# Optimization experiments

Measured on AMD Instinct MI355X. Metric: run time of the kernel, lower is better.

Reference implementation:

```python
import jax, jax.numpy as jnp
import numpy as np

EPS = 1e-6
SCALING = 32 ** -0.5  # key_dim ** -0.5


def _ln(x, g, b):
    m = jnp.mean(x, -1, keepdims=True)
    v = jnp.var(x, -1, keepdims=True)
    return (x - m) * jax.lax.rsqrt(v + EPS) * g + b


def _dwconv(x, w, b, pad):
    # x: (B,H,W,C); w: (kh,kw,1,C) depthwise kernel
    y = jax.lax.conv_general_dilated(
        x, w, (1, 1), [(pad, pad), (pad, pad)],
        dimension_numbers=("NHWC", "HWIO", "NHWC"),
        feature_group_count=x.shape[-1])
    return y + b


def _rotate_every_two(x):
    x1 = x[..., ::2]
    x2 = x[..., 1::2]
    return jnp.stack([-x2, x1], axis=-1).reshape(x.shape)


def _theta_shift(x, sin, cos):
    return x * cos + _rotate_every_two(x) * sin


def setup_inputs() -> dict:
    key = jax.random.key(0)
    ks = jax.random.split(key, 32)
    B, H, W, C = 2, 56, 56, 256
    N, D = 8, C // 8          # heads, key_dim
    F = 1024                  # ffn_dim
    L = H * W
    g = 2 ** -2.5
    inp = {
        "x": jax.random.normal(ks[0], (B, H, W, C), jnp.float32),
        "sin": jax.random.normal(ks[1], (H, W, D), jnp.float32),
        "cos": jax.random.normal(ks[2], (H, W, D), jnp.float32),
        "mask": jax.random.normal(ks[3], (N, L, L), jnp.float32),
        # pos dwconv 3x3
        "pos_w": jax.random.normal(ks[4], (3, 3, 1, C), jnp.float32) * 0.05,
        "pos_b": jnp.zeros((C,), jnp.float32),
        # retention layernorm
        "ln1_g": jnp.ones((C,), jnp.float32),
        "ln1_b": jnp.zeros((C,), jnp.float32),
        # q/k/v projections (stored as (in,out))
        "wq": jax.random.normal(ks[5], (C, C), jnp.float32) * g * (2.0 / (C + C)) ** 0.5 * 10,
        "bq": jnp.zeros((C,), jnp.float32),
        "wk": jax.random.normal(ks[6], (C, C), jnp.float32) * g * 0.06,
        "bk": jnp.zeros((C,), jnp.float32),
        "wv": jax.random.normal(ks[7], (C, C), jnp.float32) * g * 0.06,
        "bv": jnp.zeros((C,), jnp.float32),
        # lepe dwconv 5x5
        "lepe_w": jax.random.normal(ks[8], (5, 5, 1, C), jnp.float32) * 0.05,
        "lepe_b": jnp.zeros((C,), jnp.float32),
        # out proj
        "wo": jax.random.normal(ks[9], (C, C), jnp.float32) * 0.06,
        "bo": jnp.zeros((C,), jnp.float32),
        # final layernorm
        "ln2_g": jnp.ones((C,), jnp.float32),
        "ln2_b": jnp.zeros((C,), jnp.float32),
        # ffn
        "w1": jax.random.normal(ks[10], (C, F), jnp.float32) * 0.04,
        "b1": jnp.zeros((F,), jnp.float32),
        "ffn_w": jax.random.normal(ks[11], (3, 3, 1, F), jnp.float32) * 0.05,
        "ffn_b": jnp.zeros((F,), jnp.float32),
        "w2": jax.random.normal(ks[12], (F, C), jnp.float32) * 0.04,
        "b2": jnp.zeros((C,), jnp.float32),
    }
    return inp


def _forward(x, sin, cos, mask, pos_w, pos_b, ln1_g, ln1_b, wq, bq, wk, bk,
             wv, bv, lepe_w, lepe_b, wo, bo, ln2_g, ln2_b, w1, b1,
             ffn_w, ffn_b, w2, b2):
    B, H, W, C = x.shape
    N = mask.shape[0]
    D = C // N
    L = H * W

    # positional dwconv residual
    x = x + _dwconv(x, pos_w, pos_b, 1)

    # ---- retention (VisionRetentionAll) ----
    y = _ln(x, ln1_g, ln1_b)
    q = y @ wq + bq
    k = (y @ wk + bk) * SCALING
    v = y @ wv + bv
    lepe = _dwconv(v, lepe_w, lepe_b, 2)

    # (B,H,W,C) -> (B,N,H,W,D)
    q = q.reshape(B, H, W, N, D).transpose(0, 3, 1, 2, 4)
    k = k.reshape(B, H, W, N, D).transpose(0, 3, 1, 2, 4)
    qr = _theta_shift(q, sin, cos).reshape(B, N, L, D)
    kr = _theta_shift(k, sin, cos).reshape(B, N, L, D)
    vr = v.reshape(B, H, W, N, D).transpose(0, 3, 1, 2, 4).reshape(B, N, L, D)

    qk = jnp.einsum("bnld,bnmd->bnlm", qr, kr) + mask  # (B,N,L,L)
    att = jax.nn.softmax(qk, axis=-1)
    out = jnp.einsum("bnlm,bnmd->bnld", att, vr)       # (B,N,L,D)
    out = out.transpose(0, 2, 1, 3).reshape(B, H, W, C)
    out = (out + lepe) @ wo + bo
    x = x + out

    # ---- FFN with depthwise conv ----
    z = _ln(x, ln2_g, ln2_b)
    z = jax.nn.gelu(z @ w1 + b1, approximate=False)
    z = z + _dwconv(z, ffn_w, ffn_b, 1)
    z = z @ w2 + b2
    return x + z


def reference(x, sin, cos, mask, pos_w, pos_b, ln1_g, ln1_b, wq, bq, wk, bk,
              wv, bv, lepe_w, lepe_b, wo, bo, ln2_g, ln2_b, w1, b1,
              ffn_w, ffn_b, w2, b2):
    return _forward(x, sin, cos, mask, pos_w, pos_b, ln1_g, ln1_b, wq, bq,
                    wk, bk, wv, bv, lepe_w, lepe_b, wo, bo, ln2_g, ln2_b,
                    w1, b1, ffn_w, ffn_b, w2, b2)
```

## Files before the change

kernel.cpp:

```cpp
#include <hip/hip_runtime.h>
#include <hip/hip_bf16.h>
#include <math.h>

#define Bn 2
#define Hn 56
#define Wn 56
#define Cn 256
#define Nh 8
#define Dh 32
#define Fn 1024
#define Ln (Hn*Wn)
#define Mrows (Bn*Ln)
#define SCALING_K 0.17677669529663687f

typedef __attribute__((ext_vector_type(4))) float f32x4;
typedef __attribute__((ext_vector_type(8))) short s16x8;
typedef unsigned short ushort_t;

__device__ __forceinline__ ushort_t f2bf(float f) {
    __hip_bfloat16 h = __float2bfloat16(f);
    return *reinterpret_cast<ushort_t*>(&h);
}

#define GLOAD16(gp, sp) __builtin_amdgcn_global_load_lds( \
    (const __attribute__((address_space(1))) void*)(gp), \
    (__attribute__((address_space(3))) void*)(sp), 16, 0, 0)

__global__ __launch_bounds__(256) void transpose_w(
    const float* __restrict__ wq, const float* __restrict__ wk, const float* __restrict__ wv,
    const float* __restrict__ wo, const float* __restrict__ w1, const float* __restrict__ w2,
    ushort_t* __restrict__ wqkvT, ushort_t* __restrict__ woT,
    ushort_t* __restrict__ w1T, ushort_t* __restrict__ w2T)
{
    int z = blockIdx.z;
    const float* src; ushort_t* dst; int K, N; float scale = 1.f;
    switch (z) {
      case 0: src=wq; dst=wqkvT;           K=256;  N=256;  break;
      case 1: src=wk; dst=wqkvT+256*256;   K=256;  N=256;  scale=SCALING_K; break;
      case 2: src=wv; dst=wqkvT+512*256;   K=256;  N=256;  break;
      case 3: src=wo; dst=woT;             K=256;  N=256;  break;
      case 4: src=w1; dst=w1T;             K=256;  N=1024; break;
      default: src=w2; dst=w2T;            K=1024; N=256;  break;
    }
    int n0 = blockIdx.x << 5, k0 = blockIdx.y << 5;
    if (n0 >= N || k0 >= K) return;
    __shared__ float tile[32][33];
    int tx = threadIdx.x & 31, ty = threadIdx.x >> 5;
    #pragma unroll
    for (int r = 0; r < 4; ++r)
        tile[ty + 8*r][tx] = src[(size_t)(k0 + ty + 8*r)*N + n0 + tx] * scale;
    __syncthreads();
    #pragma unroll
    for (int r = 0; r < 4; ++r)
        dst[(size_t)(n0 + ty + 8*r)*K + k0 + tx] = f2bf(tile[tx][ty + 8*r]);
}

__global__ void prep_bias(const float* __restrict__ bq, const float* __restrict__ bk,
                          const float* __restrict__ bv, float* __restrict__ bqkv)
{
    int i = blockIdx.x*256 + threadIdx.x;
    if (i < 768)
        bqkv[i] = (i < 256) ? bq[i] : (i < 512 ? bk[i-256]*SCALING_K : bv[i-512]);
}

__global__ __launch_bounds__(256) void dwconv_ln(
    const float* __restrict__ x, const float* __restrict__ wgt, const float* __restrict__ bias,
    const float* __restrict__ lng, const float* __restrict__ lnb,
    float* __restrict__ out, ushort_t* __restrict__ ybf)
{
    int t = threadIdx.x;
    int cg = t & 63;
    int g = blockIdx.x*4 + (t >> 6);
    int w0 = (g % 14) << 2;
    int hr = g / 14;
    int h = hr % Hn;
    int c = cg << 2;
    float4 wv9[9];
    #pragma unroll
    for (int i = 0; i < 9; ++i) wv9[i] = *(const float4*)&wgt[i*Cn + c];
    float4 bias4 = *(const float4*)&bias[c];
    float4 acc[4] = {bias4, bias4, bias4, bias4};
    const float* base = x + (size_t)(hr - h)*Wn*Cn + c;
    #pragma unroll
    for (int dh = 0; dh < 3; ++dh) {
        int hh = h + dh - 1;
        if (hh < 0 || hh >= Hn) continue;
        const float* rowp = base + (size_t)hh*Wn*Cn;
        float4 xv[6];
        #pragma unroll
        for (int j = 0; j < 6; ++j) {
            int wc = w0 - 1 + j;
            xv[j] = (wc >= 0 && wc < Wn) ? *(const float4*)&rowp[(size_t)wc*Cn]
                                         : make_float4(0.f,0.f,0.f,0.f);
        }
        #pragma unroll
        for (int dw = 0; dw < 3; ++dw) {
            float4 wv = wv9[dh*3 + dw];
            #pragma unroll
            for (int p = 0; p < 4; ++p) {
                acc[p].x += xv[p+dw].x*wv.x; acc[p].y += xv[p+dw].y*wv.y;
                acc[p].z += xv[p+dw].z*wv.z; acc[p].w += xv[p+dw].w*wv.w;
            }
        }
        if (dh == 1) {
            #pragma unroll
            for (int p = 0; p < 4; ++p) {
                acc[p].x += xv[p+1].x; acc[p].y += xv[p+1].y;
                acc[p].z += xv[p+1].z; acc[p].w += xv[p+1].w;
            }
        }
    }
    float s[4], q[4];
    #pragma unroll
    for (int p = 0; p < 4; ++p) {
        s[p] = acc[p].x + acc[p].y + acc[p].z + acc[p].w;
        q[p] = acc[p].x*acc[p].x + acc[p].y*acc[p].y + acc[p].z*acc[p].z + acc[p].w*acc[p].w;
    }
    #pragma unroll
    for (int m = 1; m < 64; m <<= 1) {
        #pragma unroll
        for (int p = 0; p < 4; ++p) {
            s[p] += __shfl_xor(s[p], m);
            q[p] += __shfl_xor(q[p], m);
        }
    }
    float4 g4 = *(const float4*)&lng[c];
    float4 b4 = *(const float4*)&lnb[c];
    size_t pixbase = (size_t)hr*Wn + w0;
    #pragma unroll
    for (int p = 0; p < 4; ++p) {
        *(float4*)&out[(pixbase + p)*Cn + c] = acc[p];
        float mean = s[p] * (1.0f/Cn);
        float rstd = rsqrtf(q[p] * (1.0f/Cn) - mean*mean + 1e-6f);
        ushort_t o[4] = {
            f2bf((acc[p].x - mean)*rstd*g4.x + b4.x),
            f2bf((acc[p].y - mean)*rstd*g4.y + b4.y),
            f2bf((acc[p].z - mean)*rstd*g4.z + b4.z),
            f2bf((acc[p].w - mean)*rstd*g4.w + b4.w)
        };
        *(uint2*)&ybf[(pixbase + p)*Cn + c] = *(uint2*)o;
    }
}

template<int KS, int OBF>
__global__ __launch_bounds__(256) void dwconv4(
    const float* __restrict__ in, const float* __restrict__ wgt, const float* __restrict__ bias,
    void* __restrict__ outv, int C, int inld, int addin)
{
    constexpr int PAD = KS/2;
    int t = threadIdx.x;
    int cgs = C >> 2;
    int qpb = 256 / cgs;
    int cg = t % cgs;
    int g = blockIdx.x*qpb + t/cgs;
    int w0 = (g % 14) << 2;
    int hr = g / 14;
    int h = hr % Hn;
    int c = cg << 2;
    float4 bias4 = *(const float4*)&bias[c];
    float4 acc[4] = {bias4, bias4, bias4, bias4};
    const float* base = in + (size_t)(hr - h)*Wn*inld + c;
    #pragma unroll
    for (int dh = 0; dh < KS; ++dh) {
        int hh = h + dh - PAD;
        if (hh < 0 || hh >= Hn) continue;
        const float* rowp = base + (size_t)hh*Wn*inld;
        float4 xv[KS+3];
        #pragma unroll
        for (int j = 0; j < KS+3; ++j) {
            int wc = w0 - PAD + j;
            xv[j] = (wc >= 0 && wc < Wn) ? *(const float4*)&rowp[(size_t)wc*inld]
                                         : make_float4(0.f,0.f,0.f,0.f);
        }
        #pragma unroll
        for (int dw = 0; dw < KS; ++dw) {
            float4 wv = *(const float4*)&wgt[(dh*KS + dw)*C + c];
            #pragma unroll
            for (int p = 0; p < 4; ++p) {
                acc[p].x += xv[p+dw].x*wv.x; acc[p].y += xv[p+dw].y*wv.y;
                acc[p].z += xv[p+dw].z*wv.z; acc[p].w += xv[p+dw].w*wv.w;
            }
        }
        if (addin && dh == PAD) {
            #pragma unroll
            for (int p = 0; p < 4; ++p) {
                acc[p].x += xv[p+PAD].x; acc[p].y += xv[p+PAD].y;
                acc[p].z += xv[p+PAD].z; acc[p].w += xv[p+PAD].w;
            }
        }
    }
    size_t pixbase = (size_t)hr*Wn + w0;
    if (OBF) {
        ushort_t* outb = (ushort_t*)outv;
        #pragma unroll
        for (int p = 0; p < 4; ++p) {
            ushort_t tmp[4] = { f2bf(acc[p].x), f2bf(acc[p].y), f2bf(acc[p].z), f2bf(acc[p].w) };
            *(uint2*)&outb[(pixbase + p)*C + c] = *(uint2*)tmp;
        }
    } else {
        float* outf = (float*)outv;
        #pragma unroll
        for (int p = 0; p < 4; ++p)
            *(float4*)&outf[(pixbase + p)*C + c] = acc[p];
    }
}

__global__ __launch_bounds__(256) void ln_apply(
    const float* __restrict__ in, const float* __restrict__ g, const float* __restrict__ b,
    ushort_t* __restrict__ out)
{
    int t = threadIdx.x;
    int lane = t & 63;
    int row = blockIdx.x*4 + (t >> 6);
    int c = lane << 2;
    float4 v = *(const float4*)&in[(size_t)row*Cn + c];
    float s1 = v.x + v.y + v.z + v.w;
    float s2 = v.x*v.x + v.y*v.y + v.z*v.z + v.w*v.w;
    #pragma unroll
    for (int m = 1; m < 64; m <<= 1) {
        s1 += __shfl_xor(s1, m);
        s2 += __shfl_xor(s2, m);
    }
    float mean = s1 * (1.0f/Cn);
    float rstd = rsqrtf(s2 * (1.0f/Cn) - mean*mean + 1e-6f);
    float4 g4 = *(const float4*)&g[c];
    float4 b4 = *(const float4*)&b[c];
    ushort_t o[4] = {
        f2bf((v.x - mean)*rstd*g4.x + b4.x),
        f2bf((v.y - mean)*rstd*g4.y + b4.y),
        f2bf((v.z - mean)*rstd*g4.z + b4.z),
        f2bf((v.w - mean)*rstd*g4.w + b4.w)
    };
    *(uint2*)&out[(size_t)row*Cn + c] = *(uint2*)o;
}

__global__ __launch_bounds__(256) void gemm_bf16(
    const ushort_t* __restrict__ A, int lda,
    const ushort_t* __restrict__ BT, const float* __restrict__ bias,
    const float* __restrict__ resid, float* __restrict__ out, int ldo,
    int K, int gelu_flag)
{
    __shared__ __align__(16) ushort_t As[64*64];
    __shared__ __align__(16) ushort_t Bs[64*64];
    int t = threadIdx.x;
    int wid = t >> 6, lane = t & 63, l16 = lane & 15, quad = lane >> 4;
    int n0 = blockIdx.x << 6, m0 = blockIdx.y << 6;
    int rl = lane >> 3;
    int swc = ((lane & 7) ^ rl) << 3;
    const ushort_t* aA = A  + (size_t)(m0 + wid*8 + rl)*lda + swc;
    const ushort_t* aB = BT + (size_t)(n0 + wid*8 + rl)*K   + swc;
    int x7 = l16 & 7;
    f32x4 acc[4] = {{0,0,0,0},{0,0,0,0},{0,0,0,0},{0,0,0,0}};
    for (int k0 = 0; k0 < K; k0 += 64) {
        __syncthreads();
        GLOAD16(aA + k0,                 &As[wid*512]);
        GLOAD16(aA + k0 + (size_t)32*lda, &As[2048 + wid*512]);
        GLOAD16(aB + k0,                 &Bs[wid*512]);
        GLOAD16(aB + k0 + (size_t)32*K,   &Bs[2048 + wid*512]);
        __syncthreads();
        #pragma unroll
        for (int kk = 0; kk < 2; ++kk) {
            int ch = (((kk << 2) | quad) ^ x7) << 3;
            s16x8 af = *(const s16x8*)&As[(wid*16 + l16)*64 + ch];
            #pragma unroll
            for (int j = 0; j < 4; ++j) {
                s16x8 bf = *(const s16x8*)&Bs[(j*16 + l16)*64 + ch];
                acc[j] = __builtin_amdgcn_mfma_f32_16x16x32_bf16(af, bf, acc[j], 0, 0, 0);
            }
        }
    }
    #pragma unroll
    for (int j = 0; j < 4; ++j) {
        int col = n0 + j*16 + l16;
        float bv = bias[col];
        #pragma unroll
        for (int r = 0; r < 4; ++r) {
            int row = m0 + wid*16 + quad*4 + r;
            float v = acc[j][r] + bv;
            if (gelu_flag) v = 0.5f * v * (1.0f + erff(v * 0.70710678118654752f));
            size_t off = (size_t)row*ldo + col;
            if (resid) v += resid[off];
            out[off] = v;
        }
    }
}

__global__ __launch_bounds__(256) void pack_qkv(
    const float* __restrict__ qkv,
    const float* __restrict__ sp, const float* __restrict__ cp,
    ushort_t* __restrict__ qb, ushort_t* __restrict__ kb, ushort_t* __restrict__ vbT)
{
    __shared__ __align__(16) ushort_t Vl[64][40];
    int t = threadIdx.x;
    int l0 = blockIdx.x << 6;
    int n = blockIdx.y;
    int b = blockIdx.z;
    {
        int ll = t >> 2, dc = (t & 3) << 3;
        int l = l0 + ll;
        size_t gbase = ((size_t)(b*Ln + l))*768 + n*Dh + dc;
        float qx[8], kx[8], vx[8], sv[8], cv[8];
        *(float4*)&qx[0] = *(const float4*)&qkv[gbase];
        *(float4*)&qx[4] = *(const float4*)&qkv[gbase+4];
        *(float4*)&kx[0] = *(const float4*)&qkv[gbase+256];
        *(float4*)&kx[4] = *(const float4*)&qkv[gbase+260];
        *(float4*)&vx[0] = *(const float4*)&qkv[gbase+512];
        *(float4*)&vx[4] = *(const float4*)&qkv[gbase+516];
        size_t scb = (size_t)l*Dh + dc;
        *(float4*)&sv[0] = *(const float4*)&sp[scb];
        *(float4*)&sv[4] = *(const float4*)&sp[scb+4];
        *(float4*)&cv[0] = *(const float4*)&cp[scb];
        *(float4*)&cv[4] = *(const float4*)&cp[scb+4];
        ushort_t qo[8], ko[8], vo[8];
        #pragma unroll
        for (int j = 0; j < 8; j += 2) {
            float q0 = qx[j]*cv[j] - qx[j+1]*sv[j];
            float q1 = qx[j+1]*cv[j+1] + qx[j]*sv[j+1];
            float k0 = kx[j]*cv[j] - kx[j+1]*sv[j];
            float k1 = kx[j+1]*cv[j+1] + kx[j]*sv[j+1];
            qo[j] = f2bf(q0); qo[j+1] = f2bf(q1);
            ko[j] = f2bf(k0); ko[j+1] = f2bf(k1);
            vo[j] = f2bf(vx[j]); vo[j+1] = f2bf(vx[j+1]);
        }
        size_t hbase = ((size_t)((b*Nh + n)*Ln + l))*Dh + dc;
        *(uint4*)&qb[hbase] = *(uint4*)qo;
        *(uint4*)&kb[hbase] = *(uint4*)ko;
        *(uint4*)&Vl[ll][dc] = *(uint4*)vo;
    }
    __syncthreads();
    {
        int d = t >> 3, lc = (t & 7) << 3;
        ushort_t tmp[8];
        #pragma unroll
        for (int i = 0; i < 8; ++i) tmp[i] = Vl[lc + i][d];
        size_t tbase = ((size_t)((b*Nh + n)*Dh + d))*Ln + l0 + lc;
        *(uint4*)&vbT[tbase] = *(uint4*)tmp;
    }
}

__global__ __launch_bounds__(512) void flash_mfma(
    const ushort_t* __restrict__ qb, const ushort_t* __restrict__ kb,
    const ushort_t* __restrict__ vbT, const float* __restrict__ mask,
    const float* __restrict__ lepe, ushort_t* __restrict__ out)
{
    __shared__ __align__(16) ushort_t Kt[2][64][40];
    __shared__ __align__(16) ushort_t Vt[2][32][72];
    __shared__ __align__(16) ushort_t Ps[8][16][72];
    int t = threadIdx.x;
    int wid = t >> 6, lane = t & 63, l16 = lane & 15, quad = lane >> 4;
    int bb = wid & 1, wq16 = wid >> 1;
    int l0 = blockIdx.x << 6;
    int n = blockIdx.y;

    const ushort_t* qbp = qb + ((size_t)(bb*Nh + n))*Ln*Dh;
    s16x8 qfrag = *(const s16x8*)(qbp + (size_t)(l0 + wq16*16 + l16)*Dh + quad*8);
    const float* mbase = mask + (size_t)n*Ln*Ln + (size_t)(l0 + wq16*16 + quad*4)*Ln;

    int sb   = t >> 8;
    int krow = (t >> 2) & 63, kkc = (t & 3) << 3;
    int vrow = (t >> 3) & 31, vkc = (t & 7) << 3;
    const ushort_t* kst = kb  + ((size_t)(sb*Nh + n))*Ln*Dh;
    const ushort_t* vst = vbT + ((size_t)((sb*Nh + n)*Dh + vrow))*Ln;

    f32x4 O0 = {0.f,0.f,0.f,0.f}, O1 = {0.f,0.f,0.f,0.f};
    float m_[4], l_[4];
    #pragma unroll
    for (int r = 0; r < 4; ++r) { m_[r] = -INFINITY; l_[r] = 0.f; }

    uint4 kreg = *(const uint4*)(kst + (size_t)krow*Dh + kkc);
    uint4 vreg = *(const uint4*)(vst + vkc);
    f32x4 c0, c1, c2, c3;
    #pragma unroll
    for (int r = 0; r < 4; ++r) {
        const float* mr = mbase + (size_t)r*Ln + l16;
        c0[r] = mr[0]; c1[r] = mr[16]; c2[r] = mr[32]; c3[r] = mr[48];
    }

    for (int m0 = 0; m0 < Ln; m0 += 64) {
        __syncthreads();
        *(uint4*)&Kt[sb][krow][kkc] = kreg;
        *(uint4*)&Vt[sb][vrow][vkc] = vreg;
        __syncthreads();

        int m1 = m0 + 64;
        uint4 krn = kreg, vrn = vreg;
        f32x4 d0 = c0, d1 = c1, d2 = c2, d3 = c3;
        if (m1 < Ln) {
            krn = *(const uint4*)(kst + (size_t)(m1 + krow)*Dh + kkc);
            vrn = *(const uint4*)(vst + m1 + vkc);
            #pragma unroll
            for (int r = 0; r < 4; ++r) {
                const float* mr = mbase + (size_t)r*Ln + m1 + l16;
                d0[r] = mr[0]; d1[r] = mr[16]; d2[r] = mr[32]; d3[r] = mr[48];
            }
        }

        f32x4 S[4];
        {
            s16x8 kf0 = *(const s16x8*)&Kt[bb][ 0 + l16][quad*8];
            s16x8 kf1 = *(const s16x8*)&Kt[bb][16 + l16][quad*8];
            s16x8 kf2 = *(const s16x8*)&Kt[bb][32 + l16][quad*8];
            s16x8 kf3 = *(const s16x8*)&Kt[bb][48 + l16][quad*8];
            S[0] = __builtin_amdgcn_mfma_f32_16x16x32_bf16(qfrag, kf0, c0, 0, 0, 0);
            S[1] = __builtin_amdgcn_mfma_f32_16x16x32_bf16(qfrag, kf1, c1, 0, 0, 0);
            S[2] = __builtin_amdgcn_mfma_f32_16x16x32_bf16(qfrag, kf2, c2, 0, 0, 0);
            S[3] = __builtin_amdgcn_mfma_f32_16x16x32_bf16(qfrag, kf3, c3, 0, 0, 0);
        }
        #pragma unroll
        for (int r = 0; r < 4; ++r) {
            float tm = fmaxf(fmaxf(S[0][r], S[1][r]), fmaxf(S[2][r], S[3][r]));
            tm = fmaxf(tm, __shfl_xor(tm, 1));
            tm = fmaxf(tm, __shfl_xor(tm, 2));
            tm = fmaxf(tm, __shfl_xor(tm, 4));
            tm = fmaxf(tm, __shfl_xor(tm, 8));
            float nm = fmaxf(m_[r], tm);
            float al = __expf(m_[r] - nm);
            m_[r] = nm;
            float p0 = __expf(S[0][r] - nm);
            float p1 = __expf(S[1][r] - nm);
            float p2 = __expf(S[2][r] - nm);
            float p3 = __expf(S[3][r] - nm);
            float ps = p0 + p1 + p2 + p3;
            ps += __shfl_xor(ps, 1); ps += __shfl_xor(ps, 2);
            ps += __shfl_xor(ps, 4); ps += __shfl_xor(ps, 8);
            l_[r] = l_[r]*al + ps;
            O0[r] *= al; O1[r] *= al;
            int rr = quad*4 + r;
            Ps[wid][rr][ 0 + l16] = f2bf(p0);
            Ps[wid][rr][16 + l16] = f2bf(p1);
            Ps[wid][rr][32 + l16] = f2bf(p2);
            Ps[wid][rr][48 + l16] = f2bf(p3);
        }
        #pragma unroll
        for (int kc = 0; kc < 2; ++kc) {
            s16x8 pf  = *(const s16x8*)&Ps[wid][l16][kc*32 + quad*8];
            s16x8 vf0 = *(const s16x8*)&Vt[bb][ 0 + l16][kc*32 + quad*8];
            s16x8 vf1 = *(const s16x8*)&Vt[bb][16 + l16][kc*32 + quad*8];
            O0 = __builtin_amdgcn_mfma_f32_16x16x32_bf16(pf, vf0, O0, 0, 0, 0);
            O1 = __builtin_amdgcn_mfma_f32_16x16x32_bf16(pf, vf1, O1, 0, 0, 0);
        }
        kreg = krn; vreg = vrn;
        c0 = d0; c1 = d1; c2 = d2; c3 = d3;
    }
    #pragma unroll
    for (int r = 0; r < 4; ++r) {
        float inv = 1.0f / l_[r];
        size_t row = (size_t)(bb*Ln + l0 + wq16*16 + quad*4 + r)*Cn + n*Dh;
        out[row + l16]      = f2bf(O0[r] * inv + lepe[row + l16]);
        out[row + 16 + l16] = f2bf(O1[r] * inv + lepe[row + 16 + l16]);
    }
}

extern "C" void kernel_launch(void* const* d_in, const int* in_sizes, int n_in,
                              void* d_out, int out_size, void* d_ws, size_t ws_size,
                              hipStream_t stream) {
    const float* x     = (const float*)d_in[0];
    const float* sinp  = (const float*)d_in[1];
    const float* cosp  = (const float*)d_in[2];
    const float* mask  = (const float*)d_in[3];
    const float* pos_w = (const float*)d_in[4];
    const float* pos_b = (const float*)d_in[5];
    const float* ln1_g = (const float*)d_in[6];
    const float* ln1_b = (const float*)d_in[7];
    const float* wq = (const float*)d_in[8];
    const float* bq = (const float*)d_in[9];
    const float* wk = (const float*)d_in[10];
    const float* bk = (const float*)d_in[11];
    const float* wv = (const float*)d_in[12];
    const float* bv = (const float*)d_in[13];
    const float* lepe_w = (const float*)d_in[14];
    const float* lepe_b = (const float*)d_in[15];
    const float* wo = (const float*)d_in[16];
    const float* bo = (const float*)d_in[17];
    const float* ln2_g = (const float*)d_in[18];
    const float* ln2_b = (const float*)d_in[19];
    const float* w1 = (const float*)d_in[20];
    const float* b1 = (const float*)d_in[21];
    const float* ffn_w = (const float*)d_in[22];
    const float* ffn_b = (const float*)d_in[23];
    const float* w2 = (const float*)d_in[24];
    const float* b2 = (const float*)d_in[25];

    float* ws = (float*)d_ws;
    const size_t MC = (size_t)Mrows*Cn;
    const size_t HC = MC/2;
    float* xbuf = ws;
    float* x2   = ws + MC;
    float* lepe = ws + 2*MC;
    ushort_t* ybf   = (ushort_t*)(ws + 3*MC);
    ushort_t* attbf = (ushort_t*)(ws + 3*MC + HC);
    ushort_t* zbf   = (ushort_t*)(ws + 4*MC);
    float* qkv = ws + 4*MC + HC;
    ushort_t* qb  = (ushort_t*)(ws + 7*MC + HC);
    ushort_t* kb  = (ushort_t*)(ws + 8*MC);
    ushort_t* vbT = (ushort_t*)(ws + 8*MC + HC);
    float* z1 = ws + 4*MC + HC;
    ushort_t* z2bf = (ushort_t*)(ws + 9*MC);
    float* wtb = ws + 11*MC;
    ushort_t* wqkvT = (ushort_t*)wtb;
    ushort_t* woT   = (ushort_t*)(wtb + 98304);
    ushort_t* w1T   = (ushort_t*)(wtb + 131072);
    ushort_t* w2T   = (ushort_t*)(wtb + 262144);
    float*    bqkv  = wtb + 393216;
    float* outp = (float*)d_out;

    transpose_w<<<dim3(32,32,6), 256, 0, stream>>>(wq,wk,wv,wo,w1,w2, wqkvT,woT,w1T,w2T);
    prep_bias<<<3, 256, 0, stream>>>(bq,bk,bv,bqkv);
    dwconv_ln<<<Mrows/16, 256, 0, stream>>>(x, pos_w, pos_b, ln1_g, ln1_b, xbuf, ybf);
    gemm_bf16<<<dim3(12, Mrows/64), 256, 0, stream>>>(ybf, Cn,
        wqkvT, bqkv, nullptr, qkv, 768, Cn, 0);
    pack_qkv<<<dim3(Ln/64, Nh, Bn), 256, 0, stream>>>(qkv, sinp, cosp, qb, kb, vbT);
    dwconv4<5,0><<<Mrows/16, 256, 0, stream>>>(qkv+512, lepe_w, lepe_b, lepe, Cn, 768, 0);
    flash_mfma<<<dim3(Ln/64, Nh), 512, 0, stream>>>(qb, kb, vbT, mask, lepe, attbf);
    gemm_bf16<<<dim3(4, Mrows/64), 256, 0, stream>>>(attbf, Cn,
        woT, bo, xbuf, x2, Cn, Cn, 0);
    ln_apply<<<Mrows/4, 256, 0, stream>>>(x2, ln2_g, ln2_b, zbf);
    gemm_bf16<<<dim3(16, Mrows/64), 256, 0, stream>>>(zbf, Cn,
        w1T, b1, nullptr, z1, Fn, Cn, 1);
    dwconv4<3,1><<<Mrows/4, 256, 0, stream>>>(z1, ffn_w, ffn_b, z2bf, Fn, Fn, 1);
    gemm_bf16<<<dim3(4, Mrows/64), 256, 0, stream>>>(z2bf, Fn,
        w2T, b2, x2, outp, Cn, Fn, 0);
}
```

Baseline: 629.2 us.

## Fuse rotary shift and Q/K packing into QKV GEMM epilogue

The QKV GEMM epilogue now applies bias, the rotary theta shift (pairing neighbouring columns via lane shuffles) and bf16 conversion, and writes Q and K directly in per-head layout. V is written as fp32 and packed by a smaller vpack kernel, which removes the fp32 768-wide qkv round trip. The bias-prep kernel is folded into the weight-transpose launch, and the flash kernel defers its row-sum shuffle reduction to the end instead of doing it every tile. In exchange, the epilogue stores are scattered 2-byte writes and sin/cos are gathered per element.

```diff
diff --git a/kernel.cpp b/kernel.cpp
--- a/kernel.cpp
+++ b/kernel.cpp
@@ -29,10 +29,18 @@
 __global__ __launch_bounds__(256) void transpose_w(
     const float* __restrict__ wq, const float* __restrict__ wk, const float* __restrict__ wv,
     const float* __restrict__ wo, const float* __restrict__ w1, const float* __restrict__ w2,
+    const float* __restrict__ bq, const float* __restrict__ bk, const float* __restrict__ bv,
     ushort_t* __restrict__ wqkvT, ushort_t* __restrict__ woT,
-    ushort_t* __restrict__ w1T, ushort_t* __restrict__ w2T)
+    ushort_t* __restrict__ w1T, ushort_t* __restrict__ w2T, float* __restrict__ bqkv)
 {
     int z = blockIdx.z;
+    if (z == 6) {
+        if (blockIdx.x == 0 && blockIdx.y == 0) {
+            for (int i = threadIdx.x; i < 768; i += 256)
+                bqkv[i] = (i < 256) ? bq[i] : (i < 512 ? bk[i-256]*SCALING_K : bv[i-512]);
+        }
+        return;
+    }
     const float* src; ushort_t* dst; int K, N; float scale = 1.f;
     switch (z) {
       case 0: src=wq; dst=wqkvT;           K=256;  N=256;  break;
@@ -53,14 +61,6 @@
     #pragma unroll
     for (int r = 0; r < 4; ++r)
         dst[(size_t)(n0 + ty + 8*r)*K + k0 + tx] = f2bf(tile[tx][ty + 8*r]);
-}
-
-__global__ void prep_bias(const float* __restrict__ bq, const float* __restrict__ bk,
-                          const float* __restrict__ bv, float* __restrict__ bqkv)
-{
-    int i = blockIdx.x*256 + threadIdx.x;
-    if (i < 768)
-        bqkv[i] = (i < 256) ? bq[i] : (i < 512 ? bk[i-256]*SCALING_K : bv[i-512]);
 }
 
 __global__ __launch_bounds__(256) void dwconv_ln(
@@ -238,7 +238,9 @@
     const ushort_t* __restrict__ A, int lda,
     const ushort_t* __restrict__ BT, const float* __restrict__ bias,
     const float* __restrict__ resid, float* __restrict__ out, int ldo,
-    int K, int gelu_flag)
+    int K, int epi,
+    ushort_t* __restrict__ qbo, ushort_t* __restrict__ kbo, float* __restrict__ vbo,
+    const float* __restrict__ sp, const float* __restrict__ cp)
 {
     __shared__ __align__(16) ushort_t As[64*64];
     __shared__ __align__(16) ushort_t Bs[64*64];
@@ -269,6 +271,37 @@
             }
         }
     }
+    if (epi == 2) {
+        #pragma unroll
+        for (int j = 0; j < 4; ++j) {
+            int col = n0 + j*16 + l16;
+            float bv = bias[col];
+            if (col < 512) {
+                int d = col & 31;
+                int hn = (col >> 5) & 7;
+                ushort_t* dst = (col < 256) ? qbo : kbo;
+                #pragma unroll
+                for (int r = 0; r < 4; ++r) {
+                    int row = m0 + wid*16 + quad*4 + r;
+                    float v = acc[j][r] + bv;
+                    float vp = __shfl_xor(v, 1);
+                    int b = (row >= Ln) ? 1 : 0;
+                    int ll = row - b*Ln;
+                    float cc = cp[ll*Dh + d];
+                    float ss = sp[ll*Dh + d];
+                    float o = (col & 1) ? (v*cc + vp*ss) : (v*cc - vp*ss);
+                    dst[(((size_t)(b*Nh + hn)*Ln + ll) << 5) + d] = f2bf(o);
+                }
+            } else {
+                #pragma unroll
+                for (int r = 0; r < 4; ++r) {
+                    int row = m0 + wid*16 + quad*4 + r;
+                    vbo[(size_t)row*Cn + (col - 512)] = acc[j][r] + bv;
+                }
+            }
+        }
+        return;
+    }
     #pragma unroll
     for (int j = 0; j < 4; ++j) {
         int col = n0 + j*16 + l16;
@@ -277,7 +310,7 @@
         for (int r = 0; r < 4; ++r) {
             int row = m0 + wid*16 + quad*4 + r;
             float v = acc[j][r] + bv;
-            if (gelu_flag) v = 0.5f * v * (1.0f + erff(v * 0.70710678118654752f));
+            if (epi == 1) v = 0.5f * v * (1.0f + erff(v * 0.70710678118654752f));
             size_t off = (size_t)row*ldo + col;
             if (resid) v += resid[off];
             out[off] = v;
@@ -285,10 +318,8 @@
     }
 }
 
-__global__ __launch_bounds__(256) void pack_qkv(
-    const float* __restrict__ qkv,
-    const float* __restrict__ sp, const float* __restrict__ cp,
-    ushort_t* __restrict__ qb, ushort_t* __restrict__ kb, ushort_t* __restrict__ vbT)
+__global__ __launch_bounds__(256) void vpack(
+    const float* __restrict__ vbuf, ushort_t* __restrict__ vbT)
 {
     __shared__ __align__(16) ushort_t Vl[64][40];
     int t = threadIdx.x;
@@ -297,34 +328,13 @@
     int b = blockIdx.z;
     {
         int ll = t >> 2, dc = (t & 3) << 3;
-        int l = l0 + ll;
-        size_t gbase = ((size_t)(b*Ln + l))*768 + n*Dh + dc;
-        float qx[8], kx[8], vx[8], sv[8], cv[8];
-        *(float4*)&qx[0] = *(const float4*)&qkv[gbase];
-        *(float4*)&qx[4] = *(const float4*)&qkv[gbase+4];
-        *(float4*)&kx[0] = *(const float4*)&qkv[gbase+256];
-        *(float4*)&kx[4] = *(const float4*)&qkv[gbase+260];
-        *(float4*)&vx[0] = *(const float4*)&qkv[gbase+512];
-        *(float4*)&vx[4] = *(const float4*)&qkv[gbase+516];
-        size_t scb = (size_t)l*Dh + dc;
-        *(float4*)&sv[0] = *(const float4*)&sp[scb];
-        *(float4*)&sv[4] = *(const float4*)&sp[scb+4];
-        *(float4*)&cv[0] = *(const float4*)&cp[scb];
-        *(float4*)&cv[4] = *(const float4*)&cp[scb+4];
-        ushort_t qo[8], ko[8], vo[8];
-        #pragma unroll
-        for (int j = 0; j < 8; j += 2) {
-            float q0 = qx[j]*cv[j] - qx[j+1]*sv[j];
-            float q1 = qx[j+1]*cv[j+1] + qx[j]*sv[j+1];
-            float k0 = kx[j]*cv[j] - kx[j+1]*sv[j];
-            float k1 = kx[j+1]*cv[j+1] + kx[j]*sv[j+1];
-            qo[j] = f2bf(q0); qo[j+1] = f2bf(q1);
-            ko[j] = f2bf(k0); ko[j+1] = f2bf(k1);
-            vo[j] = f2bf(vx[j]); vo[j+1] = f2bf(vx[j+1]);
-        }
-        size_t hbase = ((size_t)((b*Nh + n)*Ln + l))*Dh + dc;
-        *(uint4*)&qb[hbase] = *(uint4*)qo;
-        *(uint4*)&kb[hbase] = *(uint4*)ko;
+        size_t gbase = ((size_t)(b*Ln + l0 + ll))*Cn + n*Dh + dc;
+        float vx[8];
+        *(float4*)&vx[0] = *(const float4*)&vbuf[gbase];
+        *(float4*)&vx[4] = *(const float4*)&vbuf[gbase+4];
+        ushort_t vo[8];
+        #pragma unroll
+        for (int j = 0; j < 8; ++j) vo[j] = f2bf(vx[j]);
         *(uint4*)&Vl[ll][dc] = *(uint4*)vo;
     }
     __syncthreads();
@@ -420,10 +430,7 @@
             float p1 = __expf(S[1][r] - nm);
             float p2 = __expf(S[2][r] - nm);
             float p3 = __expf(S[3][r] - nm);
-            float ps = p0 + p1 + p2 + p3;
-            ps += __shfl_xor(ps, 1); ps += __shfl_xor(ps, 2);
-            ps += __shfl_xor(ps, 4); ps += __shfl_xor(ps, 8);
-            l_[r] = l_[r]*al + ps;
+            l_[r] = l_[r]*al + (p0 + p1 + p2 + p3);
             O0[r] *= al; O1[r] *= al;
             int rr = quad*4 + r;
             Ps[wid][rr][ 0 + l16] = f2bf(p0);
@@ -444,7 +451,10 @@
     }
     #pragma unroll
     for (int r = 0; r < 4; ++r) {
-        float inv = 1.0f / l_[r];
+        float ls = l_[r];
+        ls += __shfl_xor(ls, 1); ls += __shfl_xor(ls, 2);
+        ls += __shfl_xor(ls, 4); ls += __shfl_xor(ls, 8);
+        float inv = 1.0f / ls;
         size_t row = (size_t)(bb*Ln + l0 + wq16*16 + quad*4 + r)*Cn + n*Dh;
         out[row + l16]      = f2bf(O0[r] * inv + lepe[row + l16]);
         out[row + 16 + l16] = f2bf(O1[r] * inv + lepe[row + 16 + l16]);
@@ -490,13 +500,13 @@
     ushort_t* ybf   = (ushort_t*)(ws + 3*MC);
     ushort_t* attbf = (ushort_t*)(ws + 3*MC + HC);
     ushort_t* zbf   = (ushort_t*)(ws + 4*MC);
-    float* qkv = ws + 4*MC + HC;
-    ushort_t* qb  = (ushort_t*)(ws + 7*MC + HC);
-    ushort_t* kb  = (ushort_t*)(ws + 8*MC);
-    ushort_t* vbT = (ushort_t*)(ws + 8*MC + HC);
+    float* vbuf = ws + 4*MC + HC;
+    ushort_t* qb  = (ushort_t*)(ws + 5*MC + HC);
+    ushort_t* kb  = (ushort_t*)(ws + 6*MC);
+    ushort_t* vbT = (ushort_t*)(ws + 6*MC + HC);
     float* z1 = ws + 4*MC + HC;
-    ushort_t* z2bf = (ushort_t*)(ws + 9*MC);
-    float* wtb = ws + 11*MC;
+    ushort_t* z2bf = (ushort_t*)(ws + 8*MC + HC);
+    float* wtb = ws + 10*MC + HC;
     ushort_t* wqkvT = (ushort_t*)wtb;
     ushort_t* woT   = (ushort_t*)(wtb + 98304);
     ushort_t* w1T   = (ushort_t*)(wtb + 131072);
@@ -504,20 +514,20 @@
     float*    bqkv  = wtb + 393216;
     float* outp = (float*)d_out;
 
-    transpose_w<<<dim3(32,32,6), 256, 0, stream>>>(wq,wk,wv,wo,w1,w2, wqkvT,woT,w1T,w2T);
-    prep_bias<<<3, 256, 0, stream>>>(bq,bk,bv,bqkv);
+    transpose_w<<<dim3(32,32,7), 256, 0, stream>>>(wq,wk,wv,wo,w1,w2, bq,bk,bv,
+        wqkvT,woT,w1T,w2T, bqkv);
     dwconv_ln<<<Mrows/16, 256, 0, stream>>>(x, pos_w, pos_b, ln1_g, ln1_b, xbuf, ybf);
     gemm_bf16<<<dim3(12, Mrows/64), 256, 0, stream>>>(ybf, Cn,
-        wqkvT, bqkv, nullptr, qkv, 768, Cn, 0);
-    pack_qkv<<<dim3(Ln/64, Nh, Bn), 256, 0, stream>>>(qkv, sinp, cosp, qb, kb, vbT);
-    dwconv4<5,0><<<Mrows/16, 256, 0, stream>>>(qkv+512, lepe_w, lepe_b, lepe, Cn, 768, 0);
+        wqkvT, bqkv, nullptr, nullptr, 0, Cn, 2, qb, kb, vbuf, sinp, cosp);
+    vpack<<<dim3(Ln/64, Nh, Bn), 256, 0, stream>>>(vbuf, vbT);
+    dwconv4<5,0><<<Mrows/16, 256, 0, stream>>>(vbuf, lepe_w, lepe_b, lepe, Cn, Cn, 0);
     flash_mfma<<<dim3(Ln/64, Nh), 512, 0, stream>>>(qb, kb, vbT, mask, lepe, attbf);
     gemm_bf16<<<dim3(4, Mrows/64), 256, 0, stream>>>(attbf, Cn,
-        woT, bo, xbuf, x2, Cn, Cn, 0);
+        woT, bo, xbuf, x2, Cn, Cn, 0, nullptr, nullptr, nullptr, nullptr, nullptr);
     ln_apply<<<Mrows/4, 256, 0, stream>>>(x2, ln2_g, ln2_b, zbf);
     gemm_bf16<<<dim3(16, Mrows/64), 256, 0, stream>>>(zbf, Cn,
-        w1T, b1, nullptr, z1, Fn, Cn, 1);
+        w1T, b1, nullptr, z1, Fn, Cn, 1, nullptr, nullptr, nullptr, nullptr, nullptr);
     dwconv4<3,1><<<Mrows/4, 256, 0, stream>>>(z1, ffn_w, ffn_b, z2bf, Fn, Fn, 1);
     gemm_bf16<<<dim3(4, Mrows/64), 256, 0, stream>>>(z2bf, Fn,
-        w2T, b2, x2, outp, Cn, Fn, 0);
-}
+        w2T, b2, x2, outp, Cn, Fn, 0, nullptr, nullptr, nullptr, nullptr, nullptr);
+}
```

Measured after the change: 603.6 us. -4.1%, faster.
